# Performance work log

Hardware: AMD Instinct MI355X
Metric: run time of the kernel (lower is better)

## Reference

```python
import jax, jax.numpy as jnp
import numpy as np

B, L, D, H = 8, 4096, 512, 8
DK = D // H
FACTOR = 5


def setup_inputs() -> dict:
    key = jax.random.key(0)
    ks = jax.random.split(key, 11)
    s = 0.02
    w = lambda k: (jax.random.normal(k, (D, D), jnp.float32) * s)
    b = lambda k: (jax.random.normal(k, (D,), jnp.float32) * s)
    return {
        "q": jax.random.normal(ks[0], (B, L, D), jnp.float32),
        "k": jax.random.normal(ks[1], (B, L, D), jnp.float32),
        "v": jax.random.normal(ks[2], (B, L, D), jnp.float32),
        "Wq": w(ks[3]), "bq": b(ks[4]),
        "Wk": w(ks[5]), "bk": b(ks[6]),
        "Wv": w(ks[7]), "bv": b(ks[8]),
        "Wo": w(ks[9]), "bo": b(ks[10]),
    }


def _autocorrelation(q, k, v, Wq, bq, Wk, bk, Wv, bv, Wo, bo):
    # projections -> [B, H, L, DK]
    def proj(x, W, bias):
        return (x @ W + bias).reshape(B, L, H, DK).transpose(0, 2, 1, 3)

    Q = proj(q, Wq, bq)
    K = proj(k, Wk, bk)
    V = proj(v, Wv, bv)

    # FFT-based autocorrelation along length dim
    Qf = jnp.fft.rfft(Q, axis=2)
    Kf = jnp.fft.rfft(K, axis=2)
    R = jnp.fft.irfft(Qf * jnp.conj(Kf), n=L, axis=2)  # [B, H, L, DK]

    # NOTE: this repo reduces over head then LENGTH, so topk runs over channel dim
    mean_value = R.mean(axis=(1, 2))          # [B, DK]
    mean_across_batch = mean_value.mean(axis=0)  # [DK]

    top_k = max(1, min(int(FACTOR * np.log(L)), L))
    actual_k = min(top_k, DK)                  # static: 41
    _, idx = jax.lax.top_k(mean_across_batch, actual_k)  # [k] channel-indices used as delays

    weights = jax.nn.softmax(mean_value[:, idx], axis=-1)  # [B, k]

    # top-k delay aggregation: sum_i roll(V, -idx_i, axis=2) * w_i
    t = jnp.arange(L)

    def body(acc, inp):
        d, wb = inp  # scalar delay, [B] weights
        pattern = jnp.take(V, (t + d) % L, axis=2)  # circular roll by -d
        return acc + pattern * wb[:, None, None, None], None

    agg, _ = jax.lax.scan(body, jnp.zeros_like(V), (idx, weights.T))

    out = agg.transpose(0, 2, 1, 3).reshape(B, L, D) @ Wo + bo
    return out


def reference(q, k, v, Wq, bq, Wk, bk, Wv, bv, Wo, bo):
    return _autocorrelation(q, k, v, Wq, bq, Wk, bk, Wv, bv, Wo, bo)
```

## Files before the change

kernel.cpp:

```cpp
#include <hip/hip_runtime.h>
#include <hip/hip_bf16.h>

#define LL 4096
#define DD 512
#define BB 8
#define KSEL 41

typedef __attribute__((ext_vector_type(4))) float f32x4;
typedef __attribute__((ext_vector_type(8))) short short8;

__device__ __forceinline__ ushort f2bf(float x) {
  __hip_bfloat16 h = __float2bfloat16(x);
  return *reinterpret_cast<ushort*>(&h);
}

__device__ __forceinline__ void g2lds16(const void* g, void* l) {
  __builtin_amdgcn_global_load_lds(
      (const __attribute__((address_space(1))) unsigned int*)g,
      (__attribute__((address_space(3))) unsigned int*)l, 16, 0, 0);
}

__global__ __launch_bounds__(512) void k_colsum(const float* __restrict__ q,
                                                const float* __restrict__ kk,
                                                float* __restrict__ qpart,
                                                float* __restrict__ kpart) {
  int lc = blockIdx.x, b = blockIdx.y, which = blockIdx.z;
  const float* src = which ? kk : q;
  float* part = which ? kpart : qpart;
  int c4 = (threadIdx.x & 127) * 4;
  int rg = threadIdx.x >> 7;
  float a0 = 0, a1 = 0, a2 = 0, a3 = 0;
  const float* p = src + ((size_t)b * LL + (size_t)lc * 64 + rg * 16) * DD + c4;
#pragma unroll
  for (int l = 0; l < 16; ++l) {
    float4 x = *(const float4*)(p + (size_t)l * DD);
    a0 += x.x; a1 += x.y; a2 += x.z; a3 += x.w;
  }
  float4 o = {a0, a1, a2, a3};
  *(float4*)&part[((size_t)b * 256 + lc * 4 + rg) * DD + c4] = o;
}

__global__ __launch_bounds__(256) void k_colsum2(const float* __restrict__ qpart,
                                                 const float* __restrict__ kpart,
                                                 float* __restrict__ sq,
                                                 float* __restrict__ sk) {
  int b = blockIdx.x, which = blockIdx.y;
  int c = blockIdx.z * 256 + threadIdx.x;
  const float* part = which ? kpart : qpart;
  float* dst = which ? sk : sq;
  float acc = 0.f;
#pragma unroll 8
  for (int p = 0; p < 256; ++p) acc += part[((size_t)b * 256 + p) * DD + c];
  dst[(size_t)b * DD + c] = acc;
}

__global__ __launch_bounds__(256) void k_proj(
    const float* __restrict__ sq, const float* __restrict__ sk,
    const float* __restrict__ Wq, const float* __restrict__ Wk,
    const float* __restrict__ bv, const float* __restrict__ Wo,
    float* __restrict__ partQ, float* __restrict__ partK,
    float* __restrict__ partO) {
  int jc = blockIdx.x;
  int which = blockIdx.y;
  int tid = threadIdx.x;
  int j0 = jc * 64;
  if (which == 2) {
    float a0 = 0.f, a1 = 0.f;
    for (int j = 0; j < 64; ++j) {
      float b = bv[j0 + j];
      a0 += b * Wo[(size_t)(j0 + j) * DD + tid];
      a1 += b * Wo[(size_t)(j0 + j) * DD + tid + 256];
    }
    partO[(size_t)jc * DD + tid] = a0;
    partO[(size_t)jc * DD + tid + 256] = a1;
    return;
  }
  const float* s = (which == 0) ? sq : sk;
  const float* W = (which == 0) ? Wq : Wk;
  __shared__ float ss[BB][64];
  for (int t = tid; t < BB * 64; t += 256)
    ss[t >> 6][t & 63] = s[(size_t)(t >> 6) * DD + j0 + (t & 63)];
  __syncthreads();
  float a[BB][2];
#pragma unroll
  for (int b = 0; b < BB; ++b) { a[b][0] = 0.f; a[b][1] = 0.f; }
  for (int j = 0; j < 64; ++j) {
    float w0 = W[(size_t)(j0 + j) * DD + tid];
    float w1 = W[(size_t)(j0 + j) * DD + tid + 256];
#pragma unroll
    for (int b = 0; b < BB; ++b) {
      float sv = ss[b][j];
      a[b][0] += sv * w0;
      a[b][1] += sv * w1;
    }
  }
  float* part = (which == 0) ? partQ : partK;
#pragma unroll
  for (int b = 0; b < BB; ++b) {
    part[((size_t)jc * BB + b) * DD + tid] = a[b][0];
    part[((size_t)jc * BB + b) * DD + tid + 256] = a[b][1];
  }
}

__global__ __launch_bounds__(512) void k_stats2(
    const float* __restrict__ partQ, const float* __restrict__ partK,
    const float* __restrict__ partO,
    const float* __restrict__ bq, const float* __restrict__ bk,
    const float* __restrict__ bo,
    int* __restrict__ idx_out, float* __restrict__ wts_out,
    float* __restrict__ bvo_out) {
  __shared__ float Sq[BB][DD];
  __shared__ float Sk[BB][DD];
  __shared__ float mvs[BB][64];
  __shared__ float mab[64];
  __shared__ int idxs[64];
  int tid = threadIdx.x;
  float bqv = bq[tid] * (float)LL, bkv = bk[tid] * (float)LL;
#pragma unroll
  for (int b = 0; b < BB; ++b) {
    float aq = 0.f, ak = 0.f;
#pragma unroll
    for (int jc = 0; jc < 8; ++jc) {
      aq += partQ[((size_t)jc * BB + b) * DD + tid];
      ak += partK[((size_t)jc * BB + b) * DD + tid];
    }
    Sq[b][tid] = aq + bqv;
    Sk[b][tid] = ak + bkv;
  }
  {
    float ao = 0.f;
#pragma unroll
    for (int jc = 0; jc < 8; ++jc) ao += partO[(size_t)jc * DD + tid];
    bvo_out[tid] = ao + bo[tid];
  }
  __syncthreads();
  {
    int b = tid >> 6, d = tid & 63;
    float s = 0.f;
#pragma unroll
    for (int h = 0; h < 8; ++h) s += Sq[b][h * 64 + d] * Sk[b][h * 64 + d];
    mvs[b][d] = s * (1.0f / ((float)LL * 8.0f));
  }
  __syncthreads();
  if (tid < 64) {
    float s = 0.f;
#pragma unroll
    for (int b = 0; b < BB; ++b) s += mvs[b][tid];
    mab[tid] = s * 0.125f;
  }
  __syncthreads();
  if (tid < 64) {
    float x = mab[tid];
    int r = 0;
    for (int d = 0; d < 64; ++d) {
      float y = mab[d];
      r += (y > x || (y == x && d < tid)) ? 1 : 0;
    }
    if (r < KSEL) { idxs[r] = tid; idx_out[r] = tid; }
  }
  __syncthreads();
  if (tid < BB) {
    int b = tid;
    float mx = -3.4e38f;
    for (int i = 0; i < KSEL; ++i) mx = fmaxf(mx, mvs[b][idxs[i]]);
    float s = 0.f;
    for (int i = 0; i < KSEL; ++i) s += expf(mvs[b][idxs[i]] - mx);
    float inv = 1.f / s;
    for (int i = 0; i < KSEL; ++i) wts_out[b * 64 + i] = expf(mvs[b][idxs[i]] - mx) * inv;
  }
}

__global__ __launch_bounds__(256) void k_wvot(const float* __restrict__ Wv,
                                              const float* __restrict__ Wo,
                                              ushort* __restrict__ WT) {
  __shared__ float wv[8][512];
  int tid = threadIdx.x;
  int c = blockIdx.x * 256 + tid;
  int j0 = blockIdx.y * 8;
  for (int t = tid; t < 8 * 512; t += 256)
    wv[t >> 9][t & 511] = Wv[(size_t)(j0 + (t >> 9)) * DD + (t & 511)];
  __syncthreads();
  float acc[8] = {0, 0, 0, 0, 0, 0, 0, 0};
  for (int m = 0; m < DD; ++m) {
    float wo = Wo[(size_t)m * DD + c];
#pragma unroll
    for (int j = 0; j < 8; ++j) acc[j] += wv[j][m] * wo;
  }
  ushort4 o0, o1;
  o0.x = f2bf(acc[0]); o0.y = f2bf(acc[1]); o0.z = f2bf(acc[2]); o0.w = f2bf(acc[3]);
  o1.x = f2bf(acc[4]); o1.y = f2bf(acc[5]); o1.z = f2bf(acc[6]); o1.w = f2bf(acc[7]);
  *(ushort4*)&WT[(size_t)c * DD + j0] = o0;
  *(ushort4*)&WT[(size_t)c * DD + j0 + 4] = o1;
}

__global__ __launch_bounds__(256) void k_conv(const float* __restrict__ v,
                                              const int* __restrict__ idx,
                                              const float* __restrict__ wts,
                                              ushort* __restrict__ vagg) {
  __shared__ ushort vwinT[128 * 136];
  __shared__ ushort Mlds[64 * 136];
  __shared__ float coefw[256];
  int lt = blockIdx.x;
  int ch0 = blockIdx.y * 128;
  int b = blockIdx.z;
  int tid = threadIdx.x;
  int l0 = lt * 64;

  coefw[tid] = 0.f;
  __syncthreads();
  if (tid < KSEL) coefw[64 + idx[tid]] = wts[b * 64 + tid];
  __syncthreads();

  {
    int c = tid & 127;
    int jh = tid >> 7;
    const float* vb = v + (size_t)b * LL * DD + ch0 + c;
#pragma unroll
    for (int it = 0; it < 8; ++it) {
      int j0 = (it * 2 + jh) * 8;
      union { unsigned int u[4]; short8 s; } pk;
#pragma unroll
      for (int p = 0; p < 4; ++p) {
        int ja = (l0 + j0 + 2 * p) & (LL - 1);
        int jb = (l0 + j0 + 2 * p + 1) & (LL - 1);
        float lo = vb[(size_t)ja * DD];
        float hi = vb[(size_t)jb * DD];
        pk.u[p] = (unsigned)f2bf(lo) | ((unsigned)f2bf(hi) << 16);
      }
      *(short8*)&vwinT[c * 136 + j0] = pk.s;
    }
  }
#pragma unroll
  for (int it = 0; it < 8; ++it) {
    int e = (it * 256 + tid) * 4;
    int r = e >> 7, j0 = e & 127;
    ushort4 m4;
    m4.x = f2bf(coefw[64 + j0 + 0 - r]);
    m4.y = f2bf(coefw[64 + j0 + 1 - r]);
    m4.z = f2bf(coefw[64 + j0 + 2 - r]);
    m4.w = f2bf(coefw[64 + j0 + 3 - r]);
    *(ushort4*)&Mlds[r * 136 + j0] = m4;
  }
  __syncthreads();

  int lane = tid & 63, w = tid >> 6;
  int r15 = lane & 15, g = lane >> 4;
  f32x4 acc[4][2] = {};
#pragma unroll
  for (int ks = 0; ks < 4; ++ks) {
    int kc = ks * 4 + g;
    short8 av[4], bvv[2];
#pragma unroll
    for (int m = 0; m < 4; ++m)
      av[m] = *(const short8*)&Mlds[(m * 16 + r15) * 136 + kc * 8];
#pragma unroll
    for (int n = 0; n < 2; ++n)
      bvv[n] = *(const short8*)&vwinT[(w * 32 + n * 16 + r15) * 136 + kc * 8];
#pragma unroll
    for (int m = 0; m < 4; ++m)
#pragma unroll
      for (int n = 0; n < 2; ++n)
        acc[m][n] = __builtin_amdgcn_mfma_f32_16x16x32_bf16(av[m], bvv[n], acc[m][n], 0, 0, 0);
  }

  ushort* vout = vagg + ((size_t)b * LL + l0) * DD + ch0;
#pragma unroll
  for (int m = 0; m < 4; ++m)
#pragma unroll
    for (int n = 0; n < 2; ++n)
#pragma unroll
      for (int r = 0; r < 4; ++r) {
        int row = m * 16 + g * 4 + r;
        int col = w * 32 + n * 16 + r15;
        vout[(size_t)row * DD + col] = f2bf(acc[m][n][r]);
      }
}

__global__ __launch_bounds__(256) void k_gemm(const ushort* __restrict__ A,
                                              const ushort* __restrict__ BT,
                                              const float* __restrict__ bias,
                                              float* __restrict__ C) {
  __shared__ ushort lA[128 * 64];
  __shared__ ushort lB[128 * 64];
  int bcol = blockIdx.x * 128;
  int brow = blockIdx.y * 128;
  int tid = threadIdx.x;
  int lane = tid & 63, wid = tid >> 6;
  int wr = wid >> 1, wc = wid & 1;
  int r15 = lane & 15, g = lane >> 4;
  f32x4 acc[4][4] = {};
  for (int k0 = 0; k0 < DD; k0 += 64) {
#pragma unroll
    for (int it = 0; it < 4; ++it) {
      int ch = it * 256 + tid;
      int row = ch >> 3;
      int clg = (ch & 7) ^ (row & 7);
      g2lds16(A + (size_t)(brow + row) * DD + k0 + clg * 8, &lA[ch * 8]);
      g2lds16(BT + (size_t)(bcol + row) * DD + k0 + clg * 8, &lB[ch * 8]);
    }
    asm volatile("s_waitcnt vmcnt(0)" ::: "memory");
    __syncthreads();
#pragma unroll
    for (int ks = 0; ks < 2; ++ks) {
      int kc = ks * 4 + g;
      short8 av[4], bv[4];
#pragma unroll
      for (int m = 0; m < 4; ++m) {
        int row = wr * 64 + m * 16 + r15;
        av[m] = *(const short8*)&lA[(row * 8 + (kc ^ (row & 7))) * 8];
        int col = wc * 64 + m * 16 + r15;
        bv[m] = *(const short8*)&lB[(col * 8 + (kc ^ (col & 7))) * 8];
      }
#pragma unroll
      for (int m = 0; m < 4; ++m)
#pragma unroll
        for (int n = 0; n < 4; ++n)
          acc[m][n] = __builtin_amdgcn_mfma_f32_16x16x32_bf16(av[m], bv[n], acc[m][n], 0, 0, 0);
    }
    __syncthreads();
  }
#pragma unroll
  for (int n = 0; n < 4; ++n) {
    int col = bcol + wc * 64 + n * 16 + r15;
    float bc = bias[col];
#pragma unroll
    for (int m = 0; m < 4; ++m) {
      int row = brow + wr * 64 + m * 16 + g * 4;
#pragma unroll
      for (int r = 0; r < 4; ++r)
        C[(size_t)(row + r) * DD + col] = acc[m][n][r] + bc;
    }
  }
}

extern "C" void kernel_launch(void* const* d_in, const int* in_sizes, int n_in,
                              void* d_out, int out_size, void* d_ws, size_t ws_size,
                              hipStream_t stream) {
  const float* q  = (const float*)d_in[0];
  const float* k  = (const float*)d_in[1];
  const float* v  = (const float*)d_in[2];
  const float* Wq = (const float*)d_in[3];
  const float* bq = (const float*)d_in[4];
  const float* Wk = (const float*)d_in[5];
  const float* bk = (const float*)d_in[6];
  const float* Wv = (const float*)d_in[7];
  const float* bv = (const float*)d_in[8];
  const float* Wo = (const float*)d_in[9];
  const float* bo = (const float*)d_in[10];
  float* out = (float*)d_out;

  char* ws = (char*)d_ws;
  ushort* vagg  = (ushort*)(ws + 0x0);
  ushort* wvot  = (ushort*)(ws + 0x2100000);
  float* sq     = (float*)(ws + 0x2380000);
  float* sk     = (float*)(ws + 0x2384000);
  int*   idx    = (int*)(ws + 0x2388800);
  float* wts    = (float*)(ws + 0x2388900);
  float* bvo    = (float*)(ws + 0x2389100);
  float* qpart  = (float*)(ws + 0x0);
  float* kpart  = (float*)(ws + 0x400000);
  float* partQ  = (float*)(ws + 0x2180000);
  float* partK  = (float*)(ws + 0x21A0000);
  float* partO  = (float*)(ws + 0x21C0000);

  k_colsum<<<dim3(64, 8, 2), 512, 0, stream>>>(q, k, qpart, kpart);
  k_colsum2<<<dim3(8, 2, 2), 256, 0, stream>>>(qpart, kpart, sq, sk);
  k_proj<<<dim3(8, 3), 256, 0, stream>>>(sq, sk, Wq, Wk, bv, Wo, partQ, partK, partO);
  k_stats2<<<dim3(1), 512, 0, stream>>>(partQ, partK, partO, bq, bk, bo, idx, wts, bvo);
  k_wvot<<<dim3(2, 64), 256, 0, stream>>>(Wv, Wo, wvot);
  k_conv<<<dim3(64, 4, 8), 256, 0, stream>>>(v, idx, wts, vagg);
  k_gemm<<<dim3(4, 256), 256, 0, stream>>>(vagg, wvot, bvo, out);
}
```

Before: 155.5 us.

## Fuse delay-aggregation conv and output GEMM into one kernel via LDS

Merges k_conv and k_gemm into a single 512-thread kernel. Each block computes a 64-row by 512-channel aggregated V tile with MFMA, keeps it in LDS as bf16, then multiplies it by the fused Wv·Wo matrix to write the final output. This removes the bf16 vagg round trip through global memory and one kernel launch. In exchange, LDS use of about 157KB allows only one block per CU. Every block also streams the whole 512x512 weight matrix with no double buffering, so weight reuse is lower than in the old 128x128 GEMM tiles.

```diff
diff --git a/kernel.cpp b/kernel.cpp
--- a/kernel.cpp
+++ b/kernel.cpp
@@ -193,31 +193,39 @@
   *(ushort4*)&WT[(size_t)c * DD + j0 + 4] = o1;
 }
 
-__global__ __launch_bounds__(256) void k_conv(const float* __restrict__ v,
-                                              const int* __restrict__ idx,
-                                              const float* __restrict__ wts,
-                                              ushort* __restrict__ vagg) {
-  __shared__ ushort vwinT[128 * 136];
-  __shared__ ushort Mlds[64 * 136];
-  __shared__ float coefw[256];
+struct SmP1 {
+  ushort vwinT[512 * 136];
+  ushort M[64 * 136];
+  float coefw[256];
+};
+struct SmP2 {
+  ushort vagg[64 * 520];
+  ushort lB[512 * 64];
+};
+union SmemU { SmP1 p1; SmP2 p2; };
+
+__global__ __launch_bounds__(512, 1) void k_convgemm(
+    const float* __restrict__ v, const int* __restrict__ idx,
+    const float* __restrict__ wts, const ushort* __restrict__ WvoT,
+    const float* __restrict__ bvo, float* __restrict__ C) {
+  __shared__ SmemU sm;
   int lt = blockIdx.x;
-  int ch0 = blockIdx.y * 128;
-  int b = blockIdx.z;
+  int b = blockIdx.y;
   int tid = threadIdx.x;
   int l0 = lt * 64;
-
-  coefw[tid] = 0.f;
-  __syncthreads();
-  if (tid < KSEL) coefw[64 + idx[tid]] = wts[b * 64 + tid];
-  __syncthreads();
+  int lane = tid & 63, w = tid >> 6;
+  int r15 = lane & 15, g = lane >> 4;
+
+  if (tid < 256) sm.p1.coefw[tid] = 0.f;
+  __syncthreads();
+  if (tid < KSEL) sm.p1.coefw[64 + idx[tid]] = wts[b * 64 + tid];
 
   {
-    int c = tid & 127;
-    int jh = tid >> 7;
-    const float* vb = v + (size_t)b * LL * DD + ch0 + c;
-#pragma unroll
-    for (int it = 0; it < 8; ++it) {
-      int j0 = (it * 2 + jh) * 8;
+    int c = tid;
+    const float* vb = v + (size_t)b * LL * DD + c;
+#pragma unroll
+    for (int it = 0; it < 16; ++it) {
+      int j0 = it * 8;
       union { unsigned int u[4]; short8 s; } pk;
 #pragma unroll
       for (int p = 0; p < 4; ++p) {
@@ -227,108 +235,98 @@
         float hi = vb[(size_t)jb * DD];
         pk.u[p] = (unsigned)f2bf(lo) | ((unsigned)f2bf(hi) << 16);
       }
-      *(short8*)&vwinT[c * 136 + j0] = pk.s;
-    }
-  }
-#pragma unroll
-  for (int it = 0; it < 8; ++it) {
-    int e = (it * 256 + tid) * 4;
-    int r = e >> 7, j0 = e & 127;
+      *(short8*)&sm.p1.vwinT[c * 136 + j0] = pk.s;
+    }
+  }
+  __syncthreads();
+#pragma unroll
+  for (int it = 0; it < 4; ++it) {
+    int e = it * 512 + tid;
+    int r = e >> 5, j0 = (e & 31) * 4;
     ushort4 m4;
-    m4.x = f2bf(coefw[64 + j0 + 0 - r]);
-    m4.y = f2bf(coefw[64 + j0 + 1 - r]);
-    m4.z = f2bf(coefw[64 + j0 + 2 - r]);
-    m4.w = f2bf(coefw[64 + j0 + 3 - r]);
-    *(ushort4*)&Mlds[r * 136 + j0] = m4;
-  }
-  __syncthreads();
-
-  int lane = tid & 63, w = tid >> 6;
-  int r15 = lane & 15, g = lane >> 4;
-  f32x4 acc[4][2] = {};
+    m4.x = f2bf(sm.p1.coefw[64 + j0 + 0 - r]);
+    m4.y = f2bf(sm.p1.coefw[64 + j0 + 1 - r]);
+    m4.z = f2bf(sm.p1.coefw[64 + j0 + 2 - r]);
+    m4.w = f2bf(sm.p1.coefw[64 + j0 + 3 - r]);
+    *(ushort4*)&sm.p1.M[r * 136 + j0] = m4;
+  }
+  __syncthreads();
+
+  f32x4 acc[4][4] = {};
 #pragma unroll
   for (int ks = 0; ks < 4; ++ks) {
     int kc = ks * 4 + g;
-    short8 av[4], bvv[2];
+    short8 av[4], bvv[4];
 #pragma unroll
     for (int m = 0; m < 4; ++m)
-      av[m] = *(const short8*)&Mlds[(m * 16 + r15) * 136 + kc * 8];
-#pragma unroll
-    for (int n = 0; n < 2; ++n)
-      bvv[n] = *(const short8*)&vwinT[(w * 32 + n * 16 + r15) * 136 + kc * 8];
+      av[m] = *(const short8*)&sm.p1.M[(m * 16 + r15) * 136 + kc * 8];
+#pragma unroll
+    for (int n = 0; n < 4; ++n)
+      bvv[n] = *(const short8*)&sm.p1.vwinT[(w * 64 + n * 16 + r15) * 136 + kc * 8];
 #pragma unroll
     for (int m = 0; m < 4; ++m)
 #pragma unroll
-      for (int n = 0; n < 2; ++n)
+      for (int n = 0; n < 4; ++n)
         acc[m][n] = __builtin_amdgcn_mfma_f32_16x16x32_bf16(av[m], bvv[n], acc[m][n], 0, 0, 0);
   }
-
-  ushort* vout = vagg + ((size_t)b * LL + l0) * DD + ch0;
+  __syncthreads();
+
 #pragma unroll
   for (int m = 0; m < 4; ++m)
 #pragma unroll
-    for (int n = 0; n < 2; ++n)
+    for (int n = 0; n < 4; ++n)
 #pragma unroll
       for (int r = 0; r < 4; ++r) {
         int row = m * 16 + g * 4 + r;
-        int col = w * 32 + n * 16 + r15;
-        vout[(size_t)row * DD + col] = f2bf(acc[m][n][r]);
+        int cc = w * 64 + n * 16 + r15;
+        sm.p2.vagg[row * 520 + cc] = f2bf(acc[m][n][r]);
       }
-}
-
-__global__ __launch_bounds__(256) void k_gemm(const ushort* __restrict__ A,
-                                              const ushort* __restrict__ BT,
-                                              const float* __restrict__ bias,
-                                              float* __restrict__ C) {
-  __shared__ ushort lA[128 * 64];
-  __shared__ ushort lB[128 * 64];
-  int bcol = blockIdx.x * 128;
-  int brow = blockIdx.y * 128;
-  int tid = threadIdx.x;
-  int lane = tid & 63, wid = tid >> 6;
-  int wr = wid >> 1, wc = wid & 1;
-  int r15 = lane & 15, g = lane >> 4;
-  f32x4 acc[4][4] = {};
+  __syncthreads();
+
+  f32x4 acc2[4][4] = {};
   for (int k0 = 0; k0 < DD; k0 += 64) {
 #pragma unroll
-    for (int it = 0; it < 4; ++it) {
-      int ch = it * 256 + tid;
-      int row = ch >> 3;
-      int clg = (ch & 7) ^ (row & 7);
-      g2lds16(A + (size_t)(brow + row) * DD + k0 + clg * 8, &lA[ch * 8]);
-      g2lds16(BT + (size_t)(bcol + row) * DD + k0 + clg * 8, &lB[ch * 8]);
+    for (int it = 0; it < 8; ++it) {
+      int e = it * 512 + tid;
+      int o = e >> 3;
+      int clg = (e & 7) ^ (o & 7);
+      g2lds16(WvoT + (size_t)o * DD + k0 + clg * 8, &sm.p2.lB[e * 8]);
     }
     asm volatile("s_waitcnt vmcnt(0)" ::: "memory");
     __syncthreads();
 #pragma unroll
     for (int ks = 0; ks < 2; ++ks) {
       int kc = ks * 4 + g;
-      short8 av[4], bv[4];
-#pragma unroll
-      for (int m = 0; m < 4; ++m) {
-        int row = wr * 64 + m * 16 + r15;
-        av[m] = *(const short8*)&lA[(row * 8 + (kc ^ (row & 7))) * 8];
-        int col = wc * 64 + m * 16 + r15;
-        bv[m] = *(const short8*)&lB[(col * 8 + (kc ^ (col & 7))) * 8];
+      int kk = k0 + kc * 8;
+      short8 av[4], bvv[4];
+#pragma unroll
+      for (int m = 0; m < 4; ++m)
+        av[m] = *(const short8*)&sm.p2.vagg[(m * 16 + r15) * 520 + kk];
+#pragma unroll
+      for (int n = 0; n < 4; ++n) {
+        int col = w * 64 + n * 16 + r15;
+        bvv[n] = *(const short8*)&sm.p2.lB[(col * 8 + (kc ^ (col & 7))) * 8];
       }
 #pragma unroll
       for (int m = 0; m < 4; ++m)
 #pragma unroll
         for (int n = 0; n < 4; ++n)
-          acc[m][n] = __builtin_amdgcn_mfma_f32_16x16x32_bf16(av[m], bv[n], acc[m][n], 0, 0, 0);
+          acc2[m][n] = __builtin_amdgcn_mfma_f32_16x16x32_bf16(av[m], bvv[n], acc2[m][n], 0, 0, 0);
     }
     __syncthreads();
   }
+
+  float* Cb = C + ((size_t)b * LL + l0) * DD;
 #pragma unroll
   for (int n = 0; n < 4; ++n) {
-    int col = bcol + wc * 64 + n * 16 + r15;
-    float bc = bias[col];
+    int col = w * 64 + n * 16 + r15;
+    float bc = bvo[col];
 #pragma unroll
     for (int m = 0; m < 4; ++m) {
-      int row = brow + wr * 64 + m * 16 + g * 4;
+      int row = m * 16 + g * 4;
 #pragma unroll
       for (int r = 0; r < 4; ++r)
-        C[(size_t)(row + r) * DD + col] = acc[m][n][r] + bc;
+        Cb[(size_t)(row + r) * DD + col] = acc2[m][n][r] + bc;
     }
   }
 }
@@ -350,7 +348,6 @@
   float* out = (float*)d_out;
 
   char* ws = (char*)d_ws;
-  ushort* vagg  = (ushort*)(ws + 0x0);
   ushort* wvot  = (ushort*)(ws + 0x2100000);
   float* sq     = (float*)(ws + 0x2380000);
   float* sk     = (float*)(ws + 0x2384000);
@@ -368,6 +365,5 @@
   k_proj<<<dim3(8, 3), 256, 0, stream>>>(sq, sk, Wq, Wk, bv, Wo, partQ, partK, partO);
   k_stats2<<<dim3(1), 512, 0, stream>>>(partQ, partK, partO, bq, bk, bo, idx, wts, bvo);
   k_wvot<<<dim3(2, 64), 256, 0, stream>>>(Wv, Wo, wvot);
-  k_conv<<<dim3(64, 4, 8), 256, 0, stream>>>(v, idx, wts, vagg);
-  k_gemm<<<dim3(4, 256), 256, 0, stream>>>(vagg, wvot, bvo, out);
-}
+  k_convgemm<<<dim3(64, 8), 512, 0, stream>>>(v, idx, wts, wvot, bvo, out);
+}
```

Result: slower. 174.5 us (+12.2%).
